# Kernel optimization log

Hardware: AMD Instinct MI355X
Metric: run time of the kernel (lower is better)

The kernel has to match this reference:

```python
import jax, jax.numpy as jnp
import numpy as np

NUM_SUMS = 4          # num_sums: binary vectors summed per element
BVR_LEN = 16          # group length; one 16-bit word packs one bit-vector per sum
OUT_SHAPE = (8192, 8192)  # original_data_shape (64M elements, 4M groups)
NUM_GROUPS = OUT_SHAPE[0] * OUT_SHAPE[1] // BVR_LEN
CACHE_LINES = 2 ** 16  # coeff_cache has 2^16 lines per source


def setup_inputs() -> dict:
    key = jax.random.key(0)
    k1, k2, k3 = jax.random.split(key, 3)
    coeff_cache = jax.random.normal(k1, (CACHE_LINES, NUM_SUMS), dtype=jnp.float32)
    coeff_idx = jax.random.randint(k2, (NUM_GROUPS,), 0, CACHE_LINES, dtype=jnp.int32)
    # bvr: per group, NUM_SUMS packed 16-bit words (values 0..65535 carried in int32)
    bvr = jax.random.randint(k3, (NUM_GROUPS, NUM_SUMS), 0, 65536, dtype=jnp.int32)
    return {"coeff_cache": coeff_cache, "coeff_idx": coeff_idx, "bvr": bvr}


def reference(coeff_cache, coeff_idx, bvr):
    # Unpack bits: bit l of word bvr[g, s] is the selection bit of element l
    # of group g for sum s. bits: [G, S, BVR_LEN]
    shifts = jnp.arange(BVR_LEN, dtype=bvr.dtype)
    bits = ((bvr[:, :, None] >> shifts) & 1).astype(coeff_cache.dtype)
    # Per-group coefficients via codebook gather: [G, S]
    coeff = coeff_cache[coeff_idx]
    # decoded[g, l] = sum_s coeff[g, s] * bits[g, s, l]
    # (equivalent to all_points = coeff @ bin_combs.T; decoded = all_points[coeff_sel])
    decoded = jnp.einsum("gs,gsl->gl", coeff, bits)
    return decoded.reshape(OUT_SHAPE)
```

## Files before the change

### kernel.cpp

```cpp
#include <hip/hip_runtime.h>


#define NUM_SUMS 4
#define BVR_LEN 16

typedef int   i32x4 __attribute__((ext_vector_type(4)));
typedef float f32x4 __attribute__((ext_vector_type(4)));

static constexpr int NUM_GROUPS = (8192 * 8192) / 16;
static constexpr int BLOCK      = 256;
static constexpr int G_BLK      = 256;
static constexpr int GRID       = NUM_GROUPS / G_BLK;

__global__ __launch_bounds__(BLOCK) void sbvr_decode_kernel(
        const float* __restrict__ coeff_cache,
        const int*   __restrict__ coeff_idx,
        const int*   __restrict__ bvr,
        float*       __restrict__ out)
{
    __shared__ f32x4 lds_c[G_BLK];
    __shared__ i32x4 lds_b[G_BLK];

    const int tid = threadIdx.x;
    const int g0  = blockIdx.x * G_BLK;

    {
        const int g = g0 + tid;
        const int   idx = __builtin_nontemporal_load(coeff_idx + g);
        const i32x4 b   = __builtin_nontemporal_load((const i32x4*)bvr + g);
        const f32x4 c   = ((const f32x4*)coeff_cache)[idx];
        lds_c[tid] = c;
        lds_b[tid] = b;
    }
    __syncthreads();

#pragma unroll
    for (int p = 0; p < 4; ++p) {
        const int gl = p * 64 + (tid >> 2);
        const int q4 = (tid & 3) * 4;

        const f32x4 c = lds_c[gl];
        const i32x4 b = lds_b[gl];

        f32x4 r;
#pragma unroll
        for (int j = 0; j < 4; ++j) {
            const int l = q4 + j;
            float acc = ((b.x >> l) & 1) ? c.x : 0.0f;
            acc      += ((b.y >> l) & 1) ? c.y : 0.0f;
            acc      += ((b.z >> l) & 1) ? c.z : 0.0f;
            acc      += ((b.w >> l) & 1) ? c.w : 0.0f;
            r[j] = acc;
        }
        __builtin_nontemporal_store(r, (f32x4*)out + (g0 * 4 + p * BLOCK + tid));
    }
}

extern "C" void kernel_launch(void* const* d_in, const int* in_sizes, int n_in,
                              void* d_out, int out_size, void* d_ws, size_t ws_size,
                              hipStream_t stream) {
    const float* coeff_cache = (const float*)d_in[0];
    const int*   coeff_idx   = (const int*)d_in[1];
    const int*   bvr         = (const int*)d_in[2];
    float*       out         = (float*)d_out;

    sbvr_decode_kernel<<<GRID, BLOCK, 0, stream>>>(coeff_cache, coeff_idx, bvr, out);
}
```

Measured before the change: 331.5 us.

## Use persistent blocks with double-buffered LDS prefetch of next group tile

Replaces the one-tile-per-block grid with 2048 persistent blocks, each looping over eight 256-group tiles. While the current tile is decoded and stored, the next tile's index, bvr words and gathered coefficients are loaded into registers and then written to a second LDS buffer. The goal is to hide gather latency and cut block launch overhead. In exchange there are fewer resident waves per CU and a barrier per tile, which may reduce the memory-level parallelism that many short blocks were already providing.

```diff
diff --git a/kernel.cpp b/kernel.cpp
--- a/kernel.cpp
+++ b/kernel.cpp
@@ -7,10 +7,12 @@
 typedef int   i32x4 __attribute__((ext_vector_type(4)));
 typedef float f32x4 __attribute__((ext_vector_type(4)));
 
-static constexpr int NUM_GROUPS = (8192 * 8192) / 16;
-static constexpr int BLOCK      = 256;
-static constexpr int G_BLK      = 256;
-static constexpr int GRID       = NUM_GROUPS / G_BLK;
+static constexpr int NUM_GROUPS  = (8192 * 8192) / 16;
+static constexpr int BLOCK       = 256;
+static constexpr int G_TILE      = 256;
+static constexpr int GRID        = 2048;
+static constexpr int G_PER_BLK   = NUM_GROUPS / GRID;
+static constexpr int TILES       = G_PER_BLK / G_TILE;
 
 __global__ __launch_bounds__(BLOCK) void sbvr_decode_kernel(
         const float* __restrict__ coeff_cache,
@@ -18,41 +20,57 @@
         const int*   __restrict__ bvr,
         float*       __restrict__ out)
 {
-    __shared__ f32x4 lds_c[G_BLK];
-    __shared__ i32x4 lds_b[G_BLK];
+    __shared__ f32x4 lds_c[2][G_TILE];
+    __shared__ i32x4 lds_b[2][G_TILE];
 
-    const int tid = threadIdx.x;
-    const int g0  = blockIdx.x * G_BLK;
+    const int tid   = threadIdx.x;
+    const int gbase = blockIdx.x * G_PER_BLK;
 
-    {
-        const int g = g0 + tid;
-        const int   idx = __builtin_nontemporal_load(coeff_idx + g);
-        const i32x4 b   = __builtin_nontemporal_load((const i32x4*)bvr + g);
-        const f32x4 c   = ((const f32x4*)coeff_cache)[idx];
-        lds_c[tid] = c;
-        lds_b[tid] = b;
-    }
+    int   idx = __builtin_nontemporal_load(coeff_idx + (gbase + tid));
+    i32x4 b   = __builtin_nontemporal_load((const i32x4*)bvr + (gbase + tid));
+    f32x4 c   = ((const f32x4*)coeff_cache)[idx];
+    lds_c[0][tid] = c;
+    lds_b[0][tid] = b;
     __syncthreads();
 
+#pragma unroll 1
+    for (int t = 0; t < TILES; ++t) {
+        const int cur = t & 1;
+
+        if (t + 1 < TILES) {
+            const int g = gbase + (t + 1) * G_TILE + tid;
+            idx = __builtin_nontemporal_load(coeff_idx + g);
+            b   = __builtin_nontemporal_load((const i32x4*)bvr + g);
+            c   = ((const f32x4*)coeff_cache)[idx];
+        }
+
+        const int o0 = (gbase + t * G_TILE) * 4;
 #pragma unroll
-    for (int p = 0; p < 4; ++p) {
-        const int gl = p * 64 + (tid >> 2);
-        const int q4 = (tid & 3) * 4;
+        for (int p = 0; p < 4; ++p) {
+            const int gl = p * 64 + (tid >> 2);
+            const int q4 = (tid & 3) * 4;
 
-        const f32x4 c = lds_c[gl];
-        const i32x4 b = lds_b[gl];
+            const f32x4 cc = lds_c[cur][gl];
+            const i32x4 bb = lds_b[cur][gl];
 
-        f32x4 r;
+            f32x4 r;
 #pragma unroll
-        for (int j = 0; j < 4; ++j) {
-            const int l = q4 + j;
-            float acc = ((b.x >> l) & 1) ? c.x : 0.0f;
-            acc      += ((b.y >> l) & 1) ? c.y : 0.0f;
-            acc      += ((b.z >> l) & 1) ? c.z : 0.0f;
-            acc      += ((b.w >> l) & 1) ? c.w : 0.0f;
-            r[j] = acc;
+            for (int j = 0; j < 4; ++j) {
+                const int l = q4 + j;
+                float acc = ((bb.x >> l) & 1) ? cc.x : 0.0f;
+                acc      += ((bb.y >> l) & 1) ? cc.y : 0.0f;
+                acc      += ((bb.z >> l) & 1) ? cc.z : 0.0f;
+                acc      += ((bb.w >> l) & 1) ? cc.w : 0.0f;
+                r[j] = acc;
+            }
+            __builtin_nontemporal_store(r, (f32x4*)out + (o0 + p * BLOCK + tid));
         }
-        __builtin_nontemporal_store(r, (f32x4*)out + (g0 * 4 + p * BLOCK + tid));
+
+        if (t + 1 < TILES) {
+            lds_c[cur ^ 1][tid] = c;
+            lds_b[cur ^ 1][tid] = b;
+            __syncthreads();
+        }
     }
 }
 
```

Result: no change. 337.9 us (+1.9%).
